# Performance work log

Measured on AMD Instinct MI355X. Metric: run time of the kernel, lower is better.

## Reference

```python
import jax, jax.numpy as jnp
import numpy as np

B = 8192   # batch of trajectories
T = 32     # time points
H = 256    # hidden_dim
NL = 4     # num_layers
EPS = 1e-5 # LayerNorm eps (torch default)


def setup_inputs() -> dict:
    key = jax.random.key(0)
    ks = jax.random.split(key, 8)
    # xavier-ish scales (gain 0.5 for hidden, 0.1 for output, per _init_weights)
    s0 = 0.5 * np.sqrt(2.0 / (6 + H))
    sh = 0.5 * np.sqrt(2.0 / (H + H))
    so = 0.1 * np.sqrt(2.0 / (H + 3))
    return {
        "y0": jax.random.normal(ks[0], (B, 3), dtype=jnp.float32),
        "t_span": jnp.arange(T, dtype=jnp.float32) * 0.01,
        "params": jax.random.uniform(ks[1], (B, 3), dtype=jnp.float32),  # [Omega, Delta, gamma] > 0
        "W0": jax.random.normal(ks[2], (6, H), dtype=jnp.float32) * s0,
        "b0": jnp.zeros((H,), dtype=jnp.float32),
        "Wh": jax.random.normal(ks[3], (NL - 1, H, H), dtype=jnp.float32) * sh,
        "bh": jnp.zeros((NL - 1, H), dtype=jnp.float32),
        "ln_g": jnp.ones((NL, H), dtype=jnp.float32),
        "ln_b": jnp.zeros((NL, H), dtype=jnp.float32),
        "Wout": jax.random.normal(ks[4], (H, 3), dtype=jnp.float32) * so,
        "bout": jnp.zeros((3,), dtype=jnp.float32),
        "gate": jnp.float32(0.5),
    }


def _layernorm(h, g, b):
    mu = jnp.mean(h, axis=-1, keepdims=True)
    var = jnp.mean(jnp.square(h - mu), axis=-1, keepdims=True)
    return (h - mu) * jax.lax.rsqrt(var + EPS) * g + b


def reference(y0, t_span, params, W0, b0, Wh, bh, ln_g, ln_b, Wout, bout, gate):
    def correction_net(y, p):
        # input: concat([u,v,w, Omega,Delta,gamma]) -> (B, 6)
        h = jnp.concatenate([y, p], axis=-1) @ W0 + b0
        h = jax.nn.silu(_layernorm(h, ln_g[0], ln_b[0]))
        for i in range(NL - 1):
            h = jax.nn.silu(_layernorm(h @ Wh[i] + bh[i], ln_g[i + 1], ln_b[i + 1]))
        return h @ Wout + bout  # (B, 3)

    def bloch_rhs_incomplete(y, p):
        u, v, w = y[:, 0:1], y[:, 1:2], y[:, 2:3]
        Om, ga = p[:, 0:1], p[:, 2:3]
        du = -ga * u
        dv = -ga * v - Om * w
        dw = -2.0 * ga * (w + 1.0) + Om * v
        return jnp.concatenate([du, dv, dw], axis=-1)

    def f_total(y):
        return bloch_rhs_incomplete(y, params) + gate * correction_net(y, params)

    def rk4_step(y, dt):
        k1 = f_total(y)
        k2 = f_total(y + 0.5 * dt * k1)
        k3 = f_total(y + 0.5 * dt * k2)
        k4 = f_total(y + dt * k3)
        y_new = y + (dt / 6.0) * (k1 + 2.0 * k2 + 2.0 * k3 + k4)
        return y_new, y_new

    dts = jnp.diff(t_span)              # (T-1,)
    _, ys = jax.lax.scan(rk4_step, y0, dts)
    return jnp.concatenate([y0[None], ys], axis=0)  # (T, B, 3)
```

## Files before the change

### kernel.cpp

```cpp
#include <hip/hip_runtime.h>

typedef unsigned short u16;
typedef short v8s   __attribute__((ext_vector_type(8)));
typedef float f32x4 __attribute__((ext_vector_type(4)));
typedef float f32x2 __attribute__((ext_vector_type(2)));

#define H_ 256
#define B_ 8192
#define NSTEP 31
#define NTHREADS 512
#define NBLOCKS 256
#define AROW 264

#define MFMA16(a,b,c) __builtin_amdgcn_mfma_f32_16x16x32_bf16(a,b,c,0,0,0)

#define DPP_QP_XOR1 0xB1
#define DPP_QP_XOR2 0x4E
#define DPP_ROR4    0x124
#define DPP_ROR8    0x128

template<int CTRL>
__device__ __forceinline__ float dpp_add(float v){
  return v + __int_as_float(
      __builtin_amdgcn_update_dpp(0, __float_as_int(v), CTRL, 0xF, 0xF, true));
}

__device__ __forceinline__ u16 f2bf_rne(float f){
  unsigned u = __float_as_uint(f);
  u += 0x7fffu + ((u >> 16) & 1u);
  return (u16)(u >> 16);
}
__device__ __forceinline__ u16 f2bf_trunc(float f){
  return (u16)(__float_as_uint(f) >> 16);
}

#define WS_W0   0
#define WS_W1   8192
#define WS_W23  73728
#define WS_WO   204800
#define WS_TOT  205824

__global__ void prep_kernel(const float* __restrict__ W0,
                            const float* __restrict__ b0,
                            const float* __restrict__ Wh,
                            const float* __restrict__ Wout,
                            u16* __restrict__ ws){
  int i = blockIdx.x * 256 + threadIdx.x;
  if (i < 8192){
    int q = i >> 11, n = (i >> 3) & 255, j = i & 7;
    int k = q*8 + j;
    float v = (k < 6) ? W0[k*H_ + n] : ((k == 6) ? b0[n] : 0.f);
    ws[i] = f2bf_rne(v);
  } else if (i < 73728){
    int r = i - 8192;
    int n = r >> 8, k = r & 255;
    ws[i] = f2bf_rne(Wh[k*H_ + n]);
  } else if (i < 204800){
    int r = i - 73728;
    int l = r >> 16, r2 = r & 65535;
    int kc = r2 >> 13, r3 = r2 & 8191;
    int q = r3 >> 11, n = (r3 >> 3) & 255, j = r3 & 7;
    int k = kc*32 + q*8 + j;
    ws[i] = f2bf_rne(Wh[(1 + l)*H_*H_ + k*H_ + n]);
  } else if (i < WS_TOT){
    int r = i - 204800;
    int kc = r >> 7, q = (r >> 5) & 3, nn = (r >> 3) & 3, j = r & 7;
    int k = kc*32 + q*8 + j;
    ws[i] = f2bf_rne(nn < 3 ? Wout[k*3 + nn] : 0.f);
  }
}

#define PWROW 10
#define OFF_A      0
#define OFF_W1     16896
#define OFF_WOUT   152064
#define OFF_PART   154112
#define OFF_MR     156672
#define OFF_NET    156928
#define OFF_YCUR   157440
#define OFF_YSUM   157952
#define OFF_YSTG   158464
#define OFF_P      158976
#define OFF_DTS    159488
#define LDS_TOTAL  159616

__global__ __launch_bounds__(NTHREADS, 2)
void pinode_kernel(const float* __restrict__ y0g, const float* __restrict__ t_span,
                   const float* __restrict__ params, const float* __restrict__ bhg,
                   const float* __restrict__ ln_gg, const float* __restrict__ ln_bg,
                   const float* __restrict__ boutg, const float* __restrict__ gatep,
                   const u16* __restrict__ ws, float* __restrict__ out)
{
  extern __shared__ char smem[];
  u16*   A    = (u16*)(smem + OFF_A);
  u16*   W1   = (u16*)(smem + OFF_W1);
  u16*   WO   = (u16*)(smem + OFF_WOUT);
  float* part = (float*)(smem + OFF_PART);
  float* mrs  = (float*)(smem + OFF_MR);
  float* net  = (float*)(smem + OFF_NET);
  float* ycur = (float*)(smem + OFF_YCUR);
  float* ysum = (float*)(smem + OFF_YSUM);
  float* ystg = (float*)(smem + OFF_YSTG);
  float* pL   = (float*)(smem + OFF_P);
  float* dts  = (float*)(smem + OFF_DTS);

  const int tid = threadIdx.x;
  const int wave = tid >> 6;
  const int lane = tid & 63;
  const int q    = lane >> 4;
  const int c15  = lane & 15;
  const int colbase = wave * 32;
  const int s0 = blockIdx.x * 32;

  for (int idx = tid; idx < 8192; idx += NTHREADS){
    int n = idx >> 5, ch = idx & 31;
    *(v8s*)(W1 + n*AROW + ch*8) = *(const v8s*)(ws + WS_W1 + n*256 + ch*8);
  }
  if (tid < 128)
    *(v8s*)(WO + tid*8) = *(const v8s*)(ws + WS_WO + tid*8);
  if (tid < 96){
    int s = tid & 31, c = tid >> 5;
    float y = y0g[(s0+s)*3 + c];
    ycur[s*4+c] = y; ystg[s*4+c] = y;
    pL[s*4+c]   = params[(s0+s)*3 + c];
    out[(s0+s)*3 + c] = y;
  }
  if (tid < NSTEP) dts[tid] = t_span[tid+1] - t_span[tid];

  v8s wf[2][8][2];
#pragma unroll
  for (int l = 0; l < 2; ++l)
#pragma unroll
    for (int kc = 0; kc < 8; ++kc)
#pragma unroll
      for (int nt = 0; nt < 2; ++nt)
        wf[l][kc][nt] = *(const v8s*)(ws + WS_W23 +
            (((l*8 + kc)*4 + q)*256 + colbase + nt*16 + c15)*8);

  v8s w0f[2];
#pragma unroll
  for (int nt = 0; nt < 2; ++nt)
    w0f[nt] = *(const v8s*)(ws + WS_W0 + (q*256 + colbase + nt*16 + c15)*8);

  float lng[4][2], lnb[4][2], bia[4][2];
#pragma unroll
  for (int l = 0; l < 4; ++l)
#pragma unroll
    for (int nt = 0; nt < 2; ++nt){
      int col = colbase + nt*16 + c15;
      lng[l][nt] = ln_gg[l*H_ + col];
      lnb[l][nt] = ln_bg[l*H_ + col];
      bia[l][nt] = (l == 0) ? 0.f : bhg[(l-1)*H_ + col];
    }
  const float gate = gatep[0];
  const float bo0 = boutg[0], bo1 = boutg[1], bo2 = boutg[2];
  const f32x4 fzero = {0.f, 0.f, 0.f, 0.f};

  const u16* pa  = A + c15*AROW + q*8;
  const u16* pw  = W1 + (colbase + c15)*AROW + q*8;
  u16* pstA = A + (q*4)*AROW + colbase + c15;

  __syncthreads();

  {
    int s = tid >> 4, pr = tid & 15;
    int e0 = pr*2, e1 = e0 + 1;
    float x0 = (e0 < 3) ? ystg[s*4+e0] : ((e0 < 6) ? pL[s*4+e0-3] : (e0 == 6 ? 1.f : 0.f));
    float x1 = (e1 < 3) ? ystg[s*4+e1] : ((e1 < 6) ? pL[s*4+e1-3] : (e1 == 6 ? 1.f : 0.f));
    unsigned pk = (unsigned)f2bf_rne(x0) | ((unsigned)f2bf_rne(x1) << 16);
    *(unsigned*)(A + s*AROW + e0) = pk;
  }
  __syncthreads();

  auto ln_silu = [&](f32x4 (&acc)[2][2], int li){
    float rs[2][4], rq[2][4];
#pragma unroll
    for (int mt = 0; mt < 2; ++mt)
#pragma unroll
      for (int r = 0; r < 4; ++r){
        float a0 = acc[mt][0][r], a1 = acc[mt][1][r];
        rs[mt][r] = a0 + a1;
        rq[mt][r] = a0*a0 + a1*a1;
      }
#pragma unroll
    for (int mt = 0; mt < 2; ++mt)
#pragma unroll
      for (int r = 0; r < 4; ++r){
        float s = rs[mt][r], qq = rq[mt][r];
        s = dpp_add<DPP_QP_XOR1>(s);  qq = dpp_add<DPP_QP_XOR1>(qq);
        s = dpp_add<DPP_QP_XOR2>(s);  qq = dpp_add<DPP_QP_XOR2>(qq);
        s = dpp_add<DPP_ROR4>(s);     qq = dpp_add<DPP_ROR4>(qq);
        s = dpp_add<DPP_ROR8>(s);     qq = dpp_add<DPP_ROR8>(qq);
        rs[mt][r] = s; rq[mt][r] = qq;
      }
    if (c15 == 0){
#pragma unroll
      for (int mt = 0; mt < 2; ++mt)
#pragma unroll
        for (int r = 0; r < 4; ++r){
          int row = mt*16 + q*4 + r;
          f32x2 v; v.x = rs[mt][r]; v.y = rq[mt][r];
          *(f32x2*)(part + (row*PWROW + wave)*2) = v;
        }
    }
    __syncthreads();
    if (tid < 32){
      const f32x4* pp = (const f32x4*)(part + tid*PWROW*2);
      f32x4 p0 = pp[0], p1 = pp[1], p2 = pp[2], p3 = pp[3];
      float S = p0[0]+p0[2]+p1[0]+p1[2]+p2[0]+p2[2]+p3[0]+p3[2];
      float Q = p0[1]+p0[3]+p1[1]+p1[3]+p2[1]+p2[3]+p3[1]+p3[3];
      float mean = S * (1.f/256.f);
      float var  = Q * (1.f/256.f) - mean*mean;
      float rstd = rsqrtf(var + 1e-5f);
      f32x2 mr; mr.x = rstd; mr.y = -mean*rstd;
      *(f32x2*)(mrs + tid*2) = mr;
    }
    __syncthreads();
#pragma unroll
    for (int mt = 0; mt < 2; ++mt)
#pragma unroll
      for (int r = 0; r < 4; ++r){
        int row = mt*16 + q*4 + r;
        f32x2 mr = *(const f32x2*)(mrs + row*2);
#pragma unroll
        for (int nt = 0; nt < 2; ++nt){
          float t  = acc[mt][nt][r] * mr.x + mr.y;
          float v  = t * lng[li][nt] + lnb[li][nt];
          float e  = __builtin_amdgcn_exp2f(v * -1.44269504f);
          float sv = v * __builtin_amdgcn_rcpf(1.f + e);
          pstA[(mt*16 + r)*AROW + nt*16] = f2bf_trunc(sv);
        }
      }
    __syncthreads();
  };

#pragma unroll 1
  for (int step = 0; step < NSTEP; ++step){
    float dt = dts[step];
#pragma unroll 1
    for (int stage = 0; stage < 4; ++stage){
      f32x4 acc[2][2];

#pragma unroll
      for (int mt = 0; mt < 2; ++mt)
#pragma unroll
        for (int nt = 0; nt < 2; ++nt) acc[mt][nt] = fzero;
      {
        v8s a0 = *(const v8s*)(pa);
        v8s a1 = *(const v8s*)(pa + 16*AROW);
        acc[0][0] = MFMA16(a0, w0f[0], acc[0][0]);
        acc[0][1] = MFMA16(a0, w0f[1], acc[0][1]);
        acc[1][0] = MFMA16(a1, w0f[0], acc[1][0]);
        acc[1][1] = MFMA16(a1, w0f[1], acc[1][1]);
      }
      ln_silu(acc, 0);

#pragma unroll
      for (int mt = 0; mt < 2; ++mt)
#pragma unroll
        for (int nt = 0; nt < 2; ++nt) acc[mt][nt] = fzero;
#pragma unroll
      for (int kc = 0; kc < 8; ++kc){
        v8s a0 = *(const v8s*)(pa + kc*32);
        v8s a1 = *(const v8s*)(pa + 16*AROW + kc*32);
        v8s bb0 = *(const v8s*)(pw + kc*32);
        v8s bb1 = *(const v8s*)(pw + 16*AROW + kc*32);
        acc[0][0] = MFMA16(a0, bb0, acc[0][0]);
        acc[0][1] = MFMA16(a0, bb1, acc[0][1]);
        acc[1][0] = MFMA16(a1, bb0, acc[1][0]);
        acc[1][1] = MFMA16(a1, bb1, acc[1][1]);
      }
#pragma unroll
      for (int mt = 0; mt < 2; ++mt)
#pragma unroll
        for (int nt = 0; nt < 2; ++nt)
#pragma unroll
          for (int r = 0; r < 4; ++r) acc[mt][nt][r] += bia[1][nt];
      ln_silu(acc, 1);

#pragma unroll
      for (int l = 0; l < 2; ++l){
#pragma unroll
        for (int mt = 0; mt < 2; ++mt)
#pragma unroll
          for (int nt = 0; nt < 2; ++nt) acc[mt][nt] = fzero;
#pragma unroll
        for (int kc = 0; kc < 8; ++kc){
          v8s a0 = *(const v8s*)(pa + kc*32);
          v8s a1 = *(const v8s*)(pa + 16*AROW + kc*32);
          acc[0][0] = MFMA16(a0, wf[l][kc][0], acc[0][0]);
          acc[0][1] = MFMA16(a0, wf[l][kc][1], acc[0][1]);
          acc[1][0] = MFMA16(a1, wf[l][kc][0], acc[1][0]);
          acc[1][1] = MFMA16(a1, wf[l][kc][1], acc[1][1]);
        }
#pragma unroll
        for (int mt = 0; mt < 2; ++mt)
#pragma unroll
          for (int nt = 0; nt < 2; ++nt)
#pragma unroll
            for (int r = 0; r < 4; ++r) acc[mt][nt][r] += bia[2+l][nt];
        ln_silu(acc, 2+l);
      }

      if (wave < 2){
        f32x4 ao = fzero;
        int nn = c15 < 3 ? c15 : 3;
#pragma unroll
        for (int kc = 0; kc < 8; ++kc){
          v8s a = *(const v8s*)(A + (wave*16 + c15)*AROW + kc*32 + q*8);
          v8s b = *(const v8s*)(WO + ((kc*4 + q)*4 + nn)*8);
          ao = MFMA16(a, b, ao);
        }
        if (c15 < 3){
#pragma unroll
          for (int r = 0; r < 4; ++r)
            net[(wave*16 + q*4 + r)*4 + c15] = ao[r];
        }
      }
      __syncthreads();

      if (tid < 32){
        int s = tid;
        float u = ystg[s*4+0], v = ystg[s*4+1], w = ystg[s*4+2];
        float Om = pL[s*4+0], ga = pL[s*4+2];
        float kk[3];
        kk[0] = -ga*u                      + gate*(net[s*4+0] + bo0);
        kk[1] = -ga*v - Om*w               + gate*(net[s*4+1] + bo1);
        kk[2] = -2.f*ga*(w + 1.f) + Om*v   + gate*(net[s*4+2] + bo2);
#pragma unroll
        for (int c = 0; c < 3; ++c){
          float yc = ycur[s*4+c];
          float k  = kk[c];
          float ys;
          if (stage == 3){
            float accw = ysum[s*4+c] + dt*(1.f/6.f)*k;
            ycur[s*4+c] = accw;
            ys = accw;
            out[(step+1)*(B_*3) + (s0+s)*3 + c] = accw;
          } else {
            float accw = (stage == 0) ? (yc + dt*(1.f/6.f)*k)
                                      : (ysum[s*4+c] + dt*(1.f/3.f)*k);
            ysum[s*4+c] = accw;
            ys = yc + ((stage == 2) ? dt : 0.5f*dt)*k;
          }
          ystg[s*4+c] = ys;
          A[s*AROW + c] = f2bf_rne(ys);
        }
      }
      __syncthreads();
    }
  }
}

extern "C" void kernel_launch(void* const* d_in, const int* in_sizes, int n_in,
                              void* d_out, int out_size, void* d_ws, size_t ws_size,
                              hipStream_t stream) {
  const float* y0     = (const float*)d_in[0];
  const float* t_span = (const float*)d_in[1];
  const float* params = (const float*)d_in[2];
  const float* W0     = (const float*)d_in[3];
  const float* b0     = (const float*)d_in[4];
  const float* Wh     = (const float*)d_in[5];
  const float* bh     = (const float*)d_in[6];
  const float* ln_g   = (const float*)d_in[7];
  const float* ln_b   = (const float*)d_in[8];
  const float* Wout   = (const float*)d_in[9];
  const float* bout   = (const float*)d_in[10];
  const float* gate   = (const float*)d_in[11];
  float* out = (float*)d_out;
  u16* ws = (u16*)d_ws;

  prep_kernel<<<WS_TOT/256, 256, 0, stream>>>(W0, b0, Wh, Wout, ws);

  hipFuncSetAttribute(reinterpret_cast<const void*>(pinode_kernel),
                      hipFuncAttributeMaxDynamicSharedMemorySize, LDS_TOTAL);
  pinode_kernel<<<NBLOCKS, NTHREADS, LDS_TOTAL, stream>>>(
      y0, t_span, params, bh, ln_g, ln_b, bout, gate, ws, out);
}
```

Baseline: 1.168 ms.

## Double waves per block, stream layer-3/4 weights from global, fold LN stats per wave

Raises the block to 1024 threads (16 waves), so each wave computes a 16-row by 32-column tile instead of 32x32. This cuts per-wave MFMA work and register pressure. Layers 3 and 4 no longer keep both weight sets resident in registers: one layer's fragments are prefetched from global memory during the other layer, using a reordered global layout. The separate LayerNorm reduction pass and its extra barrier are removed, so every wave reduces the row partials itself and broadcasts them with ds_bpermute. The input row is also written as one packed vector store. The trade-off is a global weight reload on every stage and more waves contending at each barrier.

```diff
diff --git a/kernel.cpp b/kernel.cpp
--- a/kernel.cpp
+++ b/kernel.cpp
@@ -8,7 +8,7 @@
 #define H_ 256
 #define B_ 8192
 #define NSTEP 31
-#define NTHREADS 512
+#define NTHREADS 1024
 #define NBLOCKS 256
 #define AROW 264
 
@@ -57,11 +57,10 @@
     ws[i] = f2bf_rne(Wh[k*H_ + n]);
   } else if (i < 204800){
     int r = i - 73728;
-    int l = r >> 16, r2 = r & 65535;
-    int kc = r2 >> 13, r3 = r2 & 8191;
-    int q = r3 >> 11, n = (r3 >> 3) & 255, j = r3 & 7;
+    int j = r & 7, kc = (r >> 3) & 7, col = (r >> 6) & 255;
+    int q = (r >> 14) & 3, l = (r >> 16) & 1;
     int k = kc*32 + q*8 + j;
-    ws[i] = f2bf_rne(Wh[(1 + l)*H_*H_ + k*H_ + n]);
+    ws[i] = f2bf_rne(Wh[(1 + l)*H_*H_ + k*H_ + col]);
   } else if (i < WS_TOT){
     int r = i - 204800;
     int kc = r >> 7, q = (r >> 5) & 3, nn = (r >> 3) & 3, j = r & 7;
@@ -70,21 +69,20 @@
   }
 }
 
-#define PWROW 10
+#define PWF 20
 #define OFF_A      0
 #define OFF_W1     16896
 #define OFF_WOUT   152064
 #define OFF_PART   154112
-#define OFF_MR     156672
-#define OFF_NET    156928
-#define OFF_YCUR   157440
-#define OFF_YSUM   157952
-#define OFF_YSTG   158464
-#define OFF_P      158976
-#define OFF_DTS    159488
-#define LDS_TOTAL  159616
-
-__global__ __launch_bounds__(NTHREADS, 2)
+#define OFF_NET    156672
+#define OFF_YCUR   157184
+#define OFF_YSUM   157696
+#define OFF_YSTG   158208
+#define OFF_P      158720
+#define OFF_DTS    159232
+#define LDS_TOTAL  159360
+
+__global__ __launch_bounds__(NTHREADS, 4)
 void pinode_kernel(const float* __restrict__ y0g, const float* __restrict__ t_span,
                    const float* __restrict__ params, const float* __restrict__ bhg,
                    const float* __restrict__ ln_gg, const float* __restrict__ ln_bg,
@@ -92,24 +90,26 @@
                    const u16* __restrict__ ws, float* __restrict__ out)
 {
   extern __shared__ char smem[];
-  u16*   A    = (u16*)(smem + OFF_A);
-  u16*   W1   = (u16*)(smem + OFF_W1);
-  u16*   WO   = (u16*)(smem + OFF_WOUT);
-  float* part = (float*)(smem + OFF_PART);
-  float* mrs  = (float*)(smem + OFF_MR);
-  float* net  = (float*)(smem + OFF_NET);
-  float* ycur = (float*)(smem + OFF_YCUR);
-  float* ysum = (float*)(smem + OFF_YSUM);
-  float* ystg = (float*)(smem + OFF_YSTG);
-  float* pL   = (float*)(smem + OFF_P);
-  float* dts  = (float*)(smem + OFF_DTS);
-
-  const int tid = threadIdx.x;
+  u16*   A     = (u16*)(smem + OFF_A);
+  u16*   W1    = (u16*)(smem + OFF_W1);
+  u16*   WO    = (u16*)(smem + OFF_WOUT);
+  float* partf = (float*)(smem + OFF_PART);
+  float* net   = (float*)(smem + OFF_NET);
+  float* ycur  = (float*)(smem + OFF_YCUR);
+  float* ysum  = (float*)(smem + OFF_YSUM);
+  float* ystg  = (float*)(smem + OFF_YSTG);
+  float* pL    = (float*)(smem + OFF_P);
+  float* dts   = (float*)(smem + OFF_DTS);
+
+  const int tid  = threadIdx.x;
   const int wave = tid >> 6;
   const int lane = tid & 63;
   const int q    = lane >> 4;
   const int c15  = lane & 15;
-  const int colbase = wave * 32;
+  const int mg   = wave & 1;
+  const int cg   = wave >> 1;
+  const int colbase = cg * 32;
+  const int rowbase = mg * 16;
   const int s0 = blockIdx.x * 32;
 
   for (int idx = tid; idx < 8192; idx += NTHREADS){
@@ -127,22 +127,14 @@
   }
   if (tid < NSTEP) dts[tid] = t_span[tid+1] - t_span[tid];
 
-  v8s wf[2][8][2];
-#pragma unroll
-  for (int l = 0; l < 2; ++l)
-#pragma unroll
-    for (int kc = 0; kc < 8; ++kc)
-#pragma unroll
-      for (int nt = 0; nt < 2; ++nt)
-        wf[l][kc][nt] = *(const v8s*)(ws + WS_W23 +
-            (((l*8 + kc)*4 + q)*256 + colbase + nt*16 + c15)*8);
-
   v8s w0f[2];
 #pragma unroll
   for (int nt = 0; nt < 2; ++nt)
     w0f[nt] = *(const v8s*)(ws + WS_W0 + (q*256 + colbase + nt*16 + c15)*8);
 
-  float lng[4][2], lnb[4][2], bia[4][2];
+  const u16* gwb = ws + WS_W23 + (q*256 + colbase + c15)*64;
+
+  float lng[4][2], lnb[4][2], bia[3][2];
 #pragma unroll
   for (int l = 0; l < 4; ++l)
 #pragma unroll
@@ -150,87 +142,88 @@
       int col = colbase + nt*16 + c15;
       lng[l][nt] = ln_gg[l*H_ + col];
       lnb[l][nt] = ln_bg[l*H_ + col];
-      bia[l][nt] = (l == 0) ? 0.f : bhg[(l-1)*H_ + col];
+      if (l >= 1) bia[l-1][nt] = bhg[(l-1)*H_ + col];
     }
   const float gate = gatep[0];
   const float bo0 = boutg[0], bo1 = boutg[1], bo2 = boutg[2];
   const f32x4 fzero = {0.f, 0.f, 0.f, 0.f};
 
-  const u16* pa  = A + c15*AROW + q*8;
-  const u16* pw  = W1 + (colbase + c15)*AROW + q*8;
-  u16* pstA = A + (q*4)*AROW + colbase + c15;
+  const u16* pa   = A + (rowbase + c15)*AROW + q*8;
+  const u16* pw   = W1 + (colbase + c15)*AROW + q*8;
+  u16*       pstA = A + (rowbase + q*4)*AROW + colbase + c15;
 
   __syncthreads();
 
-  {
-    int s = tid >> 4, pr = tid & 15;
-    int e0 = pr*2, e1 = e0 + 1;
-    float x0 = (e0 < 3) ? ystg[s*4+e0] : ((e0 < 6) ? pL[s*4+e0-3] : (e0 == 6 ? 1.f : 0.f));
-    float x1 = (e1 < 3) ? ystg[s*4+e1] : ((e1 < 6) ? pL[s*4+e1-3] : (e1 == 6 ? 1.f : 0.f));
-    unsigned pk = (unsigned)f2bf_rne(x0) | ((unsigned)f2bf_rne(x1) << 16);
-    *(unsigned*)(A + s*AROW + e0) = pk;
-  }
+  if (tid < 32){
+    int s = tid;
+    union { u16 h[8]; v8s v; } pk;
+    pk.h[0]=f2bf_rne(ystg[s*4+0]); pk.h[1]=f2bf_rne(ystg[s*4+1]); pk.h[2]=f2bf_rne(ystg[s*4+2]);
+    pk.h[3]=f2bf_rne(pL[s*4+0]);   pk.h[4]=f2bf_rne(pL[s*4+1]);   pk.h[5]=f2bf_rne(pL[s*4+2]);
+    pk.h[6]=0x3F80; pk.h[7]=0;
+    *(v8s*)(A + s*AROW) = pk.v;
+    v8s z = {0,0,0,0,0,0,0,0};
+    *(v8s*)(A + s*AROW + 8)  = z;
+    *(v8s*)(A + s*AROW + 16) = z;
+    *(v8s*)(A + s*AROW + 24) = z;
+  }
+
+  v8s wN[2][8];
+#pragma unroll
+  for (int nt = 0; nt < 2; ++nt)
+#pragma unroll
+    for (int kc = 0; kc < 8; ++kc)
+      wN[nt][kc] = *(const v8s*)(gwb + nt*1024 + kc*8);
+
   __syncthreads();
 
-  auto ln_silu = [&](f32x4 (&acc)[2][2], int li){
-    float rs[2][4], rq[2][4];
-#pragma unroll
-    for (int mt = 0; mt < 2; ++mt)
+  auto ln_silu = [&](f32x4 (&acc)[2], int li){
+    float rs[4], rq[4];
+#pragma unroll
+    for (int r = 0; r < 4; ++r){
+      float a0 = acc[0][r], a1 = acc[1][r];
+      rs[r] = a0 + a1;
+      rq[r] = a0*a0 + a1*a1;
+    }
+#pragma unroll
+    for (int r = 0; r < 4; ++r){
+      float s = rs[r], qq = rq[r];
+      s = dpp_add<DPP_QP_XOR1>(s);  qq = dpp_add<DPP_QP_XOR1>(qq);
+      s = dpp_add<DPP_QP_XOR2>(s);  qq = dpp_add<DPP_QP_XOR2>(qq);
+      s = dpp_add<DPP_ROR4>(s);     qq = dpp_add<DPP_ROR4>(qq);
+      s = dpp_add<DPP_ROR8>(s);     qq = dpp_add<DPP_ROR8>(qq);
+      rs[r] = s; rq[r] = qq;
+    }
+    if (c15 == 0){
 #pragma unroll
       for (int r = 0; r < 4; ++r){
-        float a0 = acc[mt][0][r], a1 = acc[mt][1][r];
-        rs[mt][r] = a0 + a1;
-        rq[mt][r] = a0*a0 + a1*a1;
-      }
-#pragma unroll
-    for (int mt = 0; mt < 2; ++mt)
-#pragma unroll
-      for (int r = 0; r < 4; ++r){
-        float s = rs[mt][r], qq = rq[mt][r];
-        s = dpp_add<DPP_QP_XOR1>(s);  qq = dpp_add<DPP_QP_XOR1>(qq);
-        s = dpp_add<DPP_QP_XOR2>(s);  qq = dpp_add<DPP_QP_XOR2>(qq);
-        s = dpp_add<DPP_ROR4>(s);     qq = dpp_add<DPP_ROR4>(qq);
-        s = dpp_add<DPP_ROR8>(s);     qq = dpp_add<DPP_ROR8>(qq);
-        rs[mt][r] = s; rq[mt][r] = qq;
-      }
-    if (c15 == 0){
-#pragma unroll
-      for (int mt = 0; mt < 2; ++mt)
-#pragma unroll
-        for (int r = 0; r < 4; ++r){
-          int row = mt*16 + q*4 + r;
-          f32x2 v; v.x = rs[mt][r]; v.y = rq[mt][r];
-          *(f32x2*)(part + (row*PWROW + wave)*2) = v;
-        }
+        f32x2 v; v.x = rs[r]; v.y = rq[r];
+        *(f32x2*)(partf + (rowbase + q*4 + r)*PWF + cg*2) = v;
+      }
     }
     __syncthreads();
-    if (tid < 32){
-      const f32x4* pp = (const f32x4*)(part + tid*PWROW*2);
-      f32x4 p0 = pp[0], p1 = pp[1], p2 = pp[2], p3 = pp[3];
-      float S = p0[0]+p0[2]+p1[0]+p1[2]+p2[0]+p2[2]+p3[0]+p3[2];
-      float Q = p0[1]+p0[3]+p1[1]+p1[3]+p2[1]+p2[3]+p3[1]+p3[3];
-      float mean = S * (1.f/256.f);
-      float var  = Q * (1.f/256.f) - mean*mean;
-      float rstd = rsqrtf(var + 1e-5f);
-      f32x2 mr; mr.x = rstd; mr.y = -mean*rstd;
-      *(f32x2*)(mrs + tid*2) = mr;
-    }
-    __syncthreads();
-#pragma unroll
-    for (int mt = 0; mt < 2; ++mt)
-#pragma unroll
-      for (int r = 0; r < 4; ++r){
-        int row = mt*16 + q*4 + r;
-        f32x2 mr = *(const f32x2*)(mrs + row*2);
-#pragma unroll
-        for (int nt = 0; nt < 2; ++nt){
-          float t  = acc[mt][nt][r] * mr.x + mr.y;
-          float v  = t * lng[li][nt] + lnb[li][nt];
-          float e  = __builtin_amdgcn_exp2f(v * -1.44269504f);
-          float sv = v * __builtin_amdgcn_rcpf(1.f + e);
-          pstA[(mt*16 + r)*AROW + nt*16] = f2bf_trunc(sv);
-        }
-      }
+    int r32 = lane & 31;
+    const f32x4* pp = (const f32x4*)(partf + r32*PWF);
+    f32x4 p0 = pp[0], p1 = pp[1], p2 = pp[2], p3 = pp[3];
+    float S = ((p0[0]+p0[2])+(p1[0]+p1[2]))+((p2[0]+p2[2])+(p3[0]+p3[2]));
+    float Q = ((p0[1]+p0[3])+(p1[1]+p1[3]))+((p2[1]+p2[3])+(p3[1]+p3[3]));
+    float mean = S * (1.f/256.f);
+    float var  = Q * (1.f/256.f) - mean*mean;
+    float rstd = rsqrtf(var + 1e-5f);
+    float nmr  = -mean * rstd;
+#pragma unroll
+    for (int r = 0; r < 4; ++r){
+      int row = rowbase + q*4 + r;
+      float sr = __int_as_float(__builtin_amdgcn_ds_bpermute(row << 2, __float_as_int(rstd)));
+      float sb = __int_as_float(__builtin_amdgcn_ds_bpermute(row << 2, __float_as_int(nmr)));
+#pragma unroll
+      for (int nt = 0; nt < 2; ++nt){
+        float t  = acc[nt][r] * sr + sb;
+        float v  = t * lng[li][nt] + lnb[li][nt];
+        float e  = __builtin_amdgcn_exp2f(v * -1.44269504f);
+        float sv = v * __builtin_amdgcn_rcpf(1.f + e);
+        pstA[r*AROW + nt*16] = f2bf_trunc(sv);
+      }
+    }
     __syncthreads();
   };
 
@@ -239,82 +232,80 @@
     float dt = dts[step];
 #pragma unroll 1
     for (int stage = 0; stage < 4; ++stage){
-      f32x4 acc[2][2];
-
-#pragma unroll
-      for (int mt = 0; mt < 2; ++mt)
-#pragma unroll
-        for (int nt = 0; nt < 2; ++nt) acc[mt][nt] = fzero;
+      f32x4 acc[2];
+
+      acc[0] = fzero; acc[1] = fzero;
       {
-        v8s a0 = *(const v8s*)(pa);
-        v8s a1 = *(const v8s*)(pa + 16*AROW);
-        acc[0][0] = MFMA16(a0, w0f[0], acc[0][0]);
-        acc[0][1] = MFMA16(a0, w0f[1], acc[0][1]);
-        acc[1][0] = MFMA16(a1, w0f[0], acc[1][0]);
-        acc[1][1] = MFMA16(a1, w0f[1], acc[1][1]);
+        v8s a = *(const v8s*)(pa);
+        acc[0] = MFMA16(a, w0f[0], acc[0]);
+        acc[1] = MFMA16(a, w0f[1], acc[1]);
       }
       ln_silu(acc, 0);
 
-#pragma unroll
-      for (int mt = 0; mt < 2; ++mt)
-#pragma unroll
-        for (int nt = 0; nt < 2; ++nt) acc[mt][nt] = fzero;
+      acc[0] = fzero; acc[1] = fzero;
 #pragma unroll
       for (int kc = 0; kc < 8; ++kc){
-        v8s a0 = *(const v8s*)(pa + kc*32);
-        v8s a1 = *(const v8s*)(pa + 16*AROW + kc*32);
-        v8s bb0 = *(const v8s*)(pw + kc*32);
-        v8s bb1 = *(const v8s*)(pw + 16*AROW + kc*32);
-        acc[0][0] = MFMA16(a0, bb0, acc[0][0]);
-        acc[0][1] = MFMA16(a0, bb1, acc[0][1]);
-        acc[1][0] = MFMA16(a1, bb0, acc[1][0]);
-        acc[1][1] = MFMA16(a1, bb1, acc[1][1]);
-      }
-#pragma unroll
-      for (int mt = 0; mt < 2; ++mt)
-#pragma unroll
-        for (int nt = 0; nt < 2; ++nt)
-#pragma unroll
-          for (int r = 0; r < 4; ++r) acc[mt][nt][r] += bia[1][nt];
+        v8s a  = *(const v8s*)(pa + kc*32);
+        v8s b0_ = *(const v8s*)(pw + kc*32);
+        v8s b1_ = *(const v8s*)(pw + 16*AROW + kc*32);
+        acc[0] = MFMA16(a, b0_, acc[0]);
+        acc[1] = MFMA16(a, b1_, acc[1]);
+      }
+#pragma unroll
+      for (int nt = 0; nt < 2; ++nt)
+#pragma unroll
+        for (int r = 0; r < 4; ++r) acc[nt][r] += bia[0][nt];
       ln_silu(acc, 1);
 
-#pragma unroll
-      for (int l = 0; l < 2; ++l){
-#pragma unroll
-        for (int mt = 0; mt < 2; ++mt)
-#pragma unroll
-          for (int nt = 0; nt < 2; ++nt) acc[mt][nt] = fzero;
-#pragma unroll
-        for (int kc = 0; kc < 8; ++kc){
-          v8s a0 = *(const v8s*)(pa + kc*32);
-          v8s a1 = *(const v8s*)(pa + 16*AROW + kc*32);
-          acc[0][0] = MFMA16(a0, wf[l][kc][0], acc[0][0]);
-          acc[0][1] = MFMA16(a0, wf[l][kc][1], acc[0][1]);
-          acc[1][0] = MFMA16(a1, wf[l][kc][0], acc[1][0]);
-          acc[1][1] = MFMA16(a1, wf[l][kc][1], acc[1][1]);
-        }
-#pragma unroll
-        for (int mt = 0; mt < 2; ++mt)
-#pragma unroll
-          for (int nt = 0; nt < 2; ++nt)
-#pragma unroll
-            for (int r = 0; r < 4; ++r) acc[mt][nt][r] += bia[2+l][nt];
-        ln_silu(acc, 2+l);
-      }
+      acc[0] = fzero; acc[1] = fzero;
+#pragma unroll
+      for (int kc = 0; kc < 8; ++kc){
+        v8s a = *(const v8s*)(pa + kc*32);
+        acc[0] = MFMA16(a, wN[0][kc], acc[0]);
+        acc[1] = MFMA16(a, wN[1][kc], acc[1]);
+      }
+#pragma unroll
+      for (int nt = 0; nt < 2; ++nt)
+#pragma unroll
+        for (int kc = 0; kc < 8; ++kc)
+          wN[nt][kc] = *(const v8s*)(gwb + 65536 + nt*1024 + kc*8);
+#pragma unroll
+      for (int nt = 0; nt < 2; ++nt)
+#pragma unroll
+        for (int r = 0; r < 4; ++r) acc[nt][r] += bia[1][nt];
+      ln_silu(acc, 2);
+
+      acc[0] = fzero; acc[1] = fzero;
+#pragma unroll
+      for (int kc = 0; kc < 8; ++kc){
+        v8s a = *(const v8s*)(pa + kc*32);
+        acc[0] = MFMA16(a, wN[0][kc], acc[0]);
+        acc[1] = MFMA16(a, wN[1][kc], acc[1]);
+      }
+#pragma unroll
+      for (int nt = 0; nt < 2; ++nt)
+#pragma unroll
+        for (int kc = 0; kc < 8; ++kc)
+          wN[nt][kc] = *(const v8s*)(gwb + nt*1024 + kc*8);
+#pragma unroll
+      for (int nt = 0; nt < 2; ++nt)
+#pragma unroll
+        for (int r = 0; r < 4; ++r) acc[nt][r] += bia[2][nt];
+      ln_silu(acc, 3);
 
       if (wave < 2){
         f32x4 ao = fzero;
         int nn = c15 < 3 ? c15 : 3;
 #pragma unroll
         for (int kc = 0; kc < 8; ++kc){
-          v8s a = *(const v8s*)(A + (wave*16 + c15)*AROW + kc*32 + q*8);
+          v8s a = *(const v8s*)(pa + kc*32);
           v8s b = *(const v8s*)(WO + ((kc*4 + q)*4 + nn)*8);
           ao = MFMA16(a, b, ao);
         }
         if (c15 < 3){
 #pragma unroll
           for (int r = 0; r < 4; ++r)
-            net[(wave*16 + q*4 + r)*4 + c15] = ao[r];
+            net[(rowbase + q*4 + r)*4 + c15] = ao[r];
         }
       }
       __syncthreads();
@@ -322,30 +313,34 @@
       if (tid < 32){
         int s = tid;
         float u = ystg[s*4+0], v = ystg[s*4+1], w = ystg[s*4+2];
-        float Om = pL[s*4+0], ga = pL[s*4+2];
+        float Om = pL[s*4+0], P1 = pL[s*4+1], ga = pL[s*4+2];
         float kk[3];
         kk[0] = -ga*u                      + gate*(net[s*4+0] + bo0);
         kk[1] = -ga*v - Om*w               + gate*(net[s*4+1] + bo1);
         kk[2] = -2.f*ga*(w + 1.f) + Om*v   + gate*(net[s*4+2] + bo2);
+        float ys[3];
 #pragma unroll
         for (int c = 0; c < 3; ++c){
           float yc = ycur[s*4+c];
           float k  = kk[c];
-          float ys;
           if (stage == 3){
             float accw = ysum[s*4+c] + dt*(1.f/6.f)*k;
             ycur[s*4+c] = accw;
-            ys = accw;
+            ys[c] = accw;
             out[(step+1)*(B_*3) + (s0+s)*3 + c] = accw;
           } else {
             float accw = (stage == 0) ? (yc + dt*(1.f/6.f)*k)
                                       : (ysum[s*4+c] + dt*(1.f/3.f)*k);
             ysum[s*4+c] = accw;
-            ys = yc + ((stage == 2) ? dt : 0.5f*dt)*k;
+            ys[c] = yc + ((stage == 2) ? dt : 0.5f*dt)*k;
           }
-          ystg[s*4+c] = ys;
-          A[s*AROW + c] = f2bf_rne(ys);
+          ystg[s*4+c] = ys[c];
         }
+        union { u16 h[8]; v8s v; } pk;
+        pk.h[0]=f2bf_rne(ys[0]); pk.h[1]=f2bf_rne(ys[1]); pk.h[2]=f2bf_rne(ys[2]);
+        pk.h[3]=f2bf_rne(Om);    pk.h[4]=f2bf_rne(P1);    pk.h[5]=f2bf_rne(ga);
+        pk.h[6]=0x3F80; pk.h[7]=0;
+        *(v8s*)(A + s*AROW) = pk.v;
       }
       __syncthreads();
     }
```

New measurement: 3.830 ms. 228% more time.
